# Optimization experiments

Hardware: AMD Instinct MI355X
Metric: run time of the kernel (lower is better)

## Reference

```python
import jax, jax.numpy as jnp
import numpy as np

N = 8192      # num_nodes
E = 262144    # edges (before self loops)
F_IN = 256    # input_dim
H = 4         # nheads
C = 32        # nhid (per-head out channels)
D = H * C     # concat dim = 128
NEG_SLOPE = 0.2
EPS = 1e-5


def setup_inputs() -> dict:
    key = jax.random.key(0)
    ks = jax.random.split(key, 12)
    s = 0.05
    x = jax.random.normal(ks[0], (N, F_IN), jnp.float32)
    adj = jax.random.randint(ks[1], (2, E), 0, N, dtype=jnp.int32)
    Wgat = jax.random.normal(ks[2], (F_IN, D), jnp.float32) * s   # GATConv lin weight
    att_src = jax.random.normal(ks[3], (H, C), jnp.float32) * s
    att_dst = jax.random.normal(ks[4], (H, C), jnp.float32) * s
    bias_gat = jax.random.normal(ks[5], (D,), jnp.float32) * s
    Wq = jax.random.normal(ks[6], (H, D, C), jnp.float32) * s     # per-head selfattention query proj
    Wk = jax.random.normal(ks[7], (H, D, C), jnp.float32) * s     # per-head selfattention key proj
    Wpro = jax.random.normal(ks[8], (D, D), jnp.float32) * s      # prolayer (no bias)
    ln_g = jnp.ones((D,), jnp.float32)
    ln_b = jnp.zeros((D,), jnp.float32)
    return {"x": x, "adj": adj, "Wgat": Wgat, "att_src": att_src,
            "att_dst": att_dst, "bias_gat": bias_gat, "Wq": Wq, "Wk": Wk,
            "Wpro": Wpro, "ln_g": ln_g, "ln_b": ln_b}


def _gat_conv(x, src, dst, Wgat, att_src, att_dst, bias_gat):
    # PyG GATConv, concat=True, add_self_loops handled by caller.
    xw = (x @ Wgat).reshape(N, H, C)                       # [N,H,C]
    a_src = jnp.einsum('nhc,hc->nh', xw, att_src)          # [N,H]
    a_dst = jnp.einsum('nhc,hc->nh', xw, att_dst)
    e = jax.nn.leaky_relu(a_src[src] + a_dst[dst], NEG_SLOPE)  # [Etot,H]
    # segment softmax over incoming edges of each destination node
    m = jax.ops.segment_max(e, dst, num_segments=N)        # [N,H]
    e = jnp.exp(e - m[dst])
    denom = jax.ops.segment_sum(e, dst, num_segments=N)    # [N,H]
    alpha = e / denom[dst]                                 # [Etot,H]
    out = jax.ops.segment_sum(xw[src] * alpha[:, :, None], dst, num_segments=N)
    return out.reshape(N, D) + bias_gat                    # [N,D]


def reference(x, adj, Wgat, att_src, att_dst, bias_gat, Wq, Wk, Wpro, ln_g, ln_b):
    # add self loops (PyG GATConv default)
    loops = jnp.arange(N, dtype=adj.dtype)
    src = jnp.concatenate([adj[0], loops])
    dst = jnp.concatenate([adj[1], loops])

    h_cat = _gat_conv(x, src, dst, Wgat, att_src, att_dst, bias_gat)  # [N,D]
    h = h_cat @ Wpro                                                   # prolayer

    # sum over nheads independent dense node self-attention heads
    q = jnp.einsum('nd,hdc->hnc', h, Wq)                   # [H,N,C]
    k = jnp.einsum('nd,hdc->hnc', h, Wk)
    scores = jnp.einsum('hnc,hmc->hnm', q, k) / jnp.sqrt(jnp.float32(C))  # [H,N,N]
    att = jax.nn.softmax(scores, axis=-1)
    temp = jnp.einsum('hnm,md->nd', att, h)                # sum of per-head att @ h

    y = temp + h                                           # residual
    mu = jnp.mean(y, axis=-1, keepdims=True)
    var = jnp.mean(jnp.square(y - mu), axis=-1, keepdims=True)
    return (y - mu) / jnp.sqrt(var + EPS) * ln_g + ln_b
```

## Files before the change

kernel.cpp:

```cpp
#include <hip/hip_runtime.h>
#include <math.h>

#define N_NODES 8192
#define E_EDGES 262144
#define ETOT (E_EDGES + N_NODES)
#define F_IN 256
#define NH 4
#define NC 32
#define DD 128
#define NEG_SLOPE 0.2f
#define LN_EPS 1e-5f
#define QK_SCALE (1.4426950408889634f / 5.656854249492381f)

typedef __attribute__((ext_vector_type(8))) short bf16x8;
typedef __attribute__((ext_vector_type(4))) float f32x4;

__device__ __forceinline__ float fexp2(float x) { return __builtin_amdgcn_exp2f(x); }
__device__ __forceinline__ float flog2(float x) { return __builtin_amdgcn_logf(x); }
__device__ __forceinline__ float frcp(float x)  { return __builtin_amdgcn_rcpf(x); }

__device__ __forceinline__ unsigned short f2bf(float f) {
    unsigned u = __float_as_uint(f);
    u += 0x7FFFu + ((u >> 16) & 1u);
    return (unsigned short)(u >> 16);
}
__device__ __forceinline__ unsigned pk2bf(float lo, float hi) {
    unsigned a = __float_as_uint(lo) + 0x8000u;
    unsigned b = __float_as_uint(hi) + 0x8000u;
    return __builtin_amdgcn_perm(b, a, 0x07060302u);
}

__global__ __launch_bounds__(256) void k_cvt(const float* __restrict__ Wgat,
                                             const float* __restrict__ Wpro,
                                             const float* __restrict__ Wq,
                                             const float* __restrict__ Wk,
                                             unsigned short* __restrict__ Wgt,
                                             unsigned short* __restrict__ Wpt,
                                             unsigned short* __restrict__ Wqt,
                                             unsigned short* __restrict__ Wkt) {
    int t = blockIdx.x * 256 + threadIdx.x;
    if (t < 32768) {
        int c = t >> 8, k = t & 255;
        Wgt[t] = f2bf(Wgat[(size_t)k * 128 + c]);
    } else if (t < 49152) {
        int i = t - 32768, c = i >> 7, k = i & 127;
        Wpt[i] = f2bf(Wpro[(size_t)k * 128 + c]);
    } else if (t < 65536) {
        int i = t - 49152, h = i >> 12, r = i & 4095, c = r >> 7, k = r & 127;
        Wqt[i] = f2bf(Wq[h * 4096 + k * 32 + c]);
    } else if (t < 81920) {
        int i = t - 65536, h = i >> 12, r = i & 4095, c = r >> 7, k = r & 127;
        Wkt[i] = f2bf(Wk[h * 4096 + k * 32 + c]);
    }
}

__global__ __launch_bounds__(256) void k_gemm_att(const float* __restrict__ x,
                                                  const unsigned short* __restrict__ Wgt,
                                                  const float* __restrict__ att_src,
                                                  const float* __restrict__ att_dst,
                                                  float* __restrict__ xw,
                                                  float* __restrict__ asrc,
                                                  float* __restrict__ adst) {
    __shared__ unsigned short xs[32 * 256];
    const int tid = threadIdx.x;
    const int w = tid >> 6, lane = tid & 63, lq = lane & 15, g = lane >> 4;
    const int n0 = blockIdx.x * 32;
#pragma unroll
    for (int m = 0; m < 4; ++m) {
        int lin = m * 256 + tid;
        int row = lin >> 5, ch = lin & 31;
        const float* src = &x[(size_t)(n0 + row) * 256 + ch * 8];
        float4 v0 = *(const float4*)src;
        float4 v1 = *(const float4*)(src + 4);
        uint4 o;
        o.x = (unsigned)f2bf(v0.x) | ((unsigned)f2bf(v0.y) << 16);
        o.y = (unsigned)f2bf(v0.z) | ((unsigned)f2bf(v0.w) << 16);
        o.z = (unsigned)f2bf(v1.x) | ((unsigned)f2bf(v1.y) << 16);
        o.w = (unsigned)f2bf(v1.z) | ((unsigned)f2bf(v1.w) << 16);
        *(uint4*)&xs[row * 256 + ((ch + row) & 31) * 8] = o;
    }
    __syncthreads();
    f32x4 zero = {0.f, 0.f, 0.f, 0.f};
    f32x4 acc[2][2];
#pragma unroll
    for (int s = 0; s < 2; ++s) { acc[s][0] = zero; acc[s][1] = zero; }
#pragma unroll
    for (int kb = 0; kb < 8; ++kb) {
        bf16x8 af[2], bf[2];
#pragma unroll
        for (int s = 0; s < 2; ++s) {
            int row = s * 16 + lq;
            af[s] = *(const bf16x8*)&xs[row * 256 + (((kb * 4 + g) + row) & 31) * 8];
        }
#pragma unroll
        for (int c = 0; c < 2; ++c)
            bf[c] = *(const bf16x8*)(Wgt + (size_t)(w * 32 + c * 16 + lq) * 256 + kb * 32 + g * 8);
#pragma unroll
        for (int s = 0; s < 2; ++s)
#pragma unroll
            for (int c = 0; c < 2; ++c)
                acc[s][c] = __builtin_amdgcn_mfma_f32_16x16x32_bf16(af[s], bf[c], acc[s][c], 0, 0, 0);
    }
#pragma unroll
    for (int s = 0; s < 2; ++s)
#pragma unroll
        for (int c = 0; c < 2; ++c)
#pragma unroll
            for (int r = 0; r < 4; ++r)
                xw[(size_t)(n0 + s * 16 + 4 * g + r) * DD + w * 32 + c * 16 + lq] = acc[s][c][r];
    float avs0 = att_src[w * 32 + lq],      avd0 = att_dst[w * 32 + lq];
    float avs1 = att_src[w * 32 + 16 + lq], avd1 = att_dst[w * 32 + 16 + lq];
#pragma unroll
    for (int s = 0; s < 2; ++s) {
        f32x4 vs, vd;
#pragma unroll
        for (int r = 0; r < 4; ++r) {
            vs[r] = acc[s][0][r] * avs0 + acc[s][1][r] * avs1;
            vd[r] = acc[s][0][r] * avd0 + acc[s][1][r] * avd1;
        }
#pragma unroll
        for (int off = 1; off < 16; off <<= 1)
#pragma unroll
            for (int r = 0; r < 4; ++r) {
                vs[r] += __shfl_xor(vs[r], off);
                vd[r] += __shfl_xor(vd[r], off);
            }
        if (lq == 0) {
#pragma unroll
            for (int r = 0; r < 4; ++r) {
                asrc[(n0 + s * 16 + 4 * g + r) * 4 + w] = vs[r];
                adst[(n0 + s * 16 + 4 * g + r) * 4 + w] = vd[r];
            }
        }
    }
}

__global__ __launch_bounds__(256) void k_gemm_pro(const float* __restrict__ hcat,
                                                  const unsigned short* __restrict__ Wpt,
                                                  const unsigned short* __restrict__ Wqt,
                                                  const unsigned short* __restrict__ Wkt,
                                                  float* __restrict__ hbuf,
                                                  unsigned short* __restrict__ Htb,
                                                  unsigned short* __restrict__ Qb,
                                                  unsigned short* __restrict__ Kb) {
    __shared__ unsigned short xs[32 * 128];
    __shared__ unsigned short hsd[32 * 128];
    const int tid = threadIdx.x;
    const int w = tid >> 6, lane = tid & 63, lq = lane & 15, g = lane >> 4;
    const int n0 = blockIdx.x * 32;
#pragma unroll
    for (int m = 0; m < 2; ++m) {
        int lin = m * 256 + tid;
        int row = lin >> 4, ch = lin & 15;
        const float* src = &hcat[(size_t)(n0 + row) * 128 + ch * 8];
        float4 v0 = *(const float4*)src;
        float4 v1 = *(const float4*)(src + 4);
        uint4 o;
        o.x = (unsigned)f2bf(v0.x) | ((unsigned)f2bf(v0.y) << 16);
        o.y = (unsigned)f2bf(v0.z) | ((unsigned)f2bf(v0.w) << 16);
        o.z = (unsigned)f2bf(v1.x) | ((unsigned)f2bf(v1.y) << 16);
        o.w = (unsigned)f2bf(v1.z) | ((unsigned)f2bf(v1.w) << 16);
        *(uint4*)&xs[row * 128 + ((ch + row) & 15) * 8] = o;
    }
    __syncthreads();
    f32x4 zero = {0.f, 0.f, 0.f, 0.f};
    f32x4 acc[2][2];
#pragma unroll
    for (int s = 0; s < 2; ++s) { acc[s][0] = zero; acc[s][1] = zero; }
#pragma unroll
    for (int kb = 0; kb < 4; ++kb) {
        bf16x8 af[2], bf[2];
#pragma unroll
        for (int s = 0; s < 2; ++s) {
            int row = s * 16 + lq;
            af[s] = *(const bf16x8*)&xs[row * 128 + (((kb * 4 + g) + row) & 15) * 8];
        }
#pragma unroll
        for (int c = 0; c < 2; ++c)
            bf[c] = *(const bf16x8*)(Wpt + (size_t)(w * 32 + c * 16 + lq) * 128 + kb * 32 + g * 8);
#pragma unroll
        for (int s = 0; s < 2; ++s)
#pragma unroll
            for (int c = 0; c < 2; ++c)
                acc[s][c] = __builtin_amdgcn_mfma_f32_16x16x32_bf16(af[s], bf[c], acc[s][c], 0, 0, 0);
    }
#pragma unroll
    for (int s = 0; s < 2; ++s)
#pragma unroll
        for (int c = 0; c < 2; ++c) {
            int col = w * 32 + c * 16 + lq;
#pragma unroll
            for (int r = 0; r < 4; ++r) {
                int row = s * 16 + 4 * g + r;
                hbuf[(size_t)(n0 + row) * 128 + col] = acc[s][c][r];
                hsd[row * 128 + (((col >> 3) + row) & 15) * 8 + (col & 7)] = f2bf(acc[s][c][r]);
            }
            uint2 hp;
            hp.x = pk2bf(acc[s][c][0], acc[s][c][1]);
            hp.y = pk2bf(acc[s][c][2], acc[s][c][3]);
            *(uint2*)(Htb + (size_t)col * N_NODES + n0 + s * 16 + 4 * g) = hp;
        }
    __syncthreads();
    f32x4 aq[2][2], ak[2][2];
#pragma unroll
    for (int s = 0; s < 2; ++s)
#pragma unroll
        for (int c = 0; c < 2; ++c) { aq[s][c] = zero; ak[s][c] = zero; }
#pragma unroll
    for (int kb = 0; kb < 4; ++kb) {
        bf16x8 af[2], bq[2], bk[2];
#pragma unroll
        for (int s = 0; s < 2; ++s) {
            int row = s * 16 + lq;
            af[s] = *(const bf16x8*)&hsd[row * 128 + (((kb * 4 + g) + row) & 15) * 8];
        }
#pragma unroll
        for (int c = 0; c < 2; ++c) {
            size_t widx = ((size_t)w * 32 + c * 16 + lq) * 128 + kb * 32 + g * 8;
            bq[c] = *(const bf16x8*)(Wqt + widx);
            bk[c] = *(const bf16x8*)(Wkt + widx);
        }
#pragma unroll
        for (int s = 0; s < 2; ++s)
#pragma unroll
            for (int c = 0; c < 2; ++c) {
                aq[s][c] = __builtin_amdgcn_mfma_f32_16x16x32_bf16(af[s], bq[c], aq[s][c], 0, 0, 0);
                ak[s][c] = __builtin_amdgcn_mfma_f32_16x16x32_bf16(af[s], bk[c], ak[s][c], 0, 0, 0);
            }
    }
#pragma unroll
    for (int s = 0; s < 2; ++s)
#pragma unroll
        for (int c = 0; c < 2; ++c)
#pragma unroll
            for (int r = 0; r < 4; ++r) {
                size_t nidx = (size_t)w * N_NODES + n0 + s * 16 + 4 * g + r;
                Qb[nidx * NC + c * 16 + lq] = f2bf(aq[s][c][r] * QK_SCALE);
                Kb[nidx * NC + c * 16 + lq] = f2bf(ak[s][c][r]);
            }
}

__device__ __forceinline__ void edge_sd(int e, const int* adj, int& s, int& d) {
    if (e < E_EDGES) { s = adj[e]; d = adj[E_EDGES + e]; }
    else { s = e - E_EDGES; d = s; }
}

__global__ void k_deg(const int* __restrict__ adj, int* __restrict__ deg) {
    int e = blockIdx.x * blockDim.x + threadIdx.x;
    if (e >= ETOT) return;
    int d = (e < E_EDGES) ? adj[E_EDGES + e] : e - E_EDGES;
    atomicAdd(&deg[d], 1);
}

__global__ __launch_bounds__(1024) void k_scan(const int* __restrict__ deg,
                                               int* __restrict__ rowptr,
                                               int* __restrict__ cursor) {
    __shared__ int sm[1024];
    int t = threadIdx.x;
    int v[8], sum = 0;
#pragma unroll
    for (int j = 0; j < 8; ++j) { v[j] = deg[t * 8 + j]; sum += v[j]; }
    sm[t] = sum;
    __syncthreads();
    for (int off = 1; off < 1024; off <<= 1) {
        int x = (t >= off) ? sm[t - off] : 0;
        __syncthreads();
        sm[t] += x;
        __syncthreads();
    }
    int base = sm[t] - sum;
#pragma unroll
    for (int j = 0; j < 8; ++j) {
        rowptr[t * 8 + j] = base;
        cursor[t * 8 + j] = base;
        base += v[j];
    }
    if (t == 1023) rowptr[8192] = base;
}

__global__ void k_fill(const int* __restrict__ adj, const float* __restrict__ asrc,
                       const float* __restrict__ adst, int* __restrict__ cursor,
                       uint4* __restrict__ rec_csr) {
    int e = blockIdx.x * blockDim.x + threadIdx.x;
    if (e >= ETOT) return;
    int s, d; edge_sd(e, adj, s, d);
    int pos = atomicAdd(&cursor[d], 1);
    float4 as4 = *(const float4*)&asrc[s * 4];
    float4 ad4 = *(const float4*)&adst[d * 4];
    const float L2E = 1.4426950408889634f;
    float v;
    float4 p;
    v = as4.x + ad4.x; v = v > 0.f ? v : NEG_SLOPE * v; p.x = fexp2(v * L2E);
    v = as4.y + ad4.y; v = v > 0.f ? v : NEG_SLOPE * v; p.y = fexp2(v * L2E);
    v = as4.z + ad4.z; v = v > 0.f ? v : NEG_SLOPE * v; p.z = fexp2(v * L2E);
    v = as4.w + ad4.w; v = v > 0.f ? v : NEG_SLOPE * v; p.w = fexp2(v * L2E);
    uint4 rec;
    rec.x = (unsigned)s;
    rec.y = pk2bf(p.x, p.y);
    rec.z = pk2bf(p.z, p.w);
    rec.w = 0u;
    rec_csr[pos] = rec;
}

__global__ __launch_bounds__(256) void k_aggregate(const int* __restrict__ rowptr,
                                                   const uint4* __restrict__ rec_csr,
                                                   const float* __restrict__ xw,
                                                   const float* __restrict__ bias,
                                                   float* __restrict__ hcat) {
    int n = blockIdx.x * 2 + (threadIdx.x >> 7);
    int c = threadIdx.x & 127;
    int h = c >> 5;
    int beg = rowptr[n], end = rowptr[n + 1];
    float acc = 0.f, den = 0.f;
    int i = beg;
    for (; i + 2 <= end; i += 2) {
        uint4 r0 = rec_csr[i], r1 = rec_csr[i + 1];
        unsigned w0 = (h < 2) ? r0.y : r0.z;
        unsigned w1 = (h < 2) ? r1.y : r1.z;
        float p0 = __uint_as_float((h & 1) ? (w0 & 0xFFFF0000u) : (w0 << 16));
        float p1 = __uint_as_float((h & 1) ? (w1 & 0xFFFF0000u) : (w1 << 16));
        den += p0 + p1;
        acc += p0 * xw[(size_t)r0.x * DD + c] + p1 * xw[(size_t)r1.x * DD + c];
    }
    if (i < end) {
        uint4 r0 = rec_csr[i];
        unsigned w0 = (h < 2) ? r0.y : r0.z;
        float p0 = __uint_as_float((h & 1) ? (w0 & 0xFFFF0000u) : (w0 << 16));
        den += p0;
        acc += p0 * xw[(size_t)r0.x * DD + c];
    }
    hcat[(size_t)n * DD + c] = bias[c] + acc * frcp(den);
}

__global__ __launch_bounds__(256) void k_attn_l(const unsigned short* __restrict__ Qb,
                                                const unsigned short* __restrict__ Kb,
                                                float* __restrict__ lsum) {
    const int tid = threadIdx.x;
    const int w = tid >> 6;
    const int lane = tid & 63;
    const int lq = lane & 15;
    const int g = lane >> 4;
    const int q0 = blockIdx.x * 64;
    const int ks = blockIdx.y;
    f32x4 zero = {0.f, 0.f, 0.f, 0.f};

    bf16x8 qf[4];
#pragma unroll
    for (int j = 0; j < 4; ++j)
        qf[j] = *(const bf16x8*)(Qb + ((size_t)w * N_NODES + q0 + j * 16 + lq) * NC + g * 8);
    const unsigned short* Kp = Kb + (size_t)w * N_NODES * NC;

    float l[4] = {0.f, 0.f, 0.f, 0.f};
    for (int kt = 0; kt < 16; ++kt) {
        const int k0 = ks * 1024 + kt * 64;
#pragma unroll
        for (int t = 0; t < 4; ++t) {
            const bf16x8 kf = *(const bf16x8*)(Kp + (size_t)(k0 + t * 16 + lq) * NC + g * 8);
#pragma unroll
            for (int j = 0; j < 4; ++j) {
                f32x4 st = __builtin_amdgcn_mfma_f32_16x16x32_bf16(kf, qf[j], zero, 0, 0, 0);
                l[j] += (fexp2(st[0]) + fexp2(st[1])) + (fexp2(st[2]) + fexp2(st[3]));
            }
        }
    }
#pragma unroll
    for (int j = 0; j < 4; ++j) {
        float lj = l[j];
        lj += __shfl_xor(lj, 16); lj += __shfl_xor(lj, 32);
        if (lane < 16) atomicAdd(&lsum[w * N_NODES + q0 + j * 16 + lq], lj);
    }
}

__global__ __launch_bounds__(256, 2) void k_attn_pv(
        const unsigned short* __restrict__ Qb,
        const unsigned short* __restrict__ Kb,
        const unsigned short* __restrict__ Htb,
        const float* __restrict__ lsum,
        float* __restrict__ Opart) {
    __shared__ unsigned short htl[128 * 64];
    __shared__ unsigned short plds[32 * 64];
    const int tid = threadIdx.x;
    const int w = tid >> 6;
    const int lane = tid & 63;
    const int lq = lane & 15;
    const int g = lane >> 4;
    const int q0 = blockIdx.x * 32;
    const int ks = blockIdx.y;
    const int sd = tid >> 3, sc = tid & 7;
    f32x4 zero = {0.f, 0.f, 0.f, 0.f};

    float lg0[4], lg1[4];
    bf16x8 qreg0[4], qreg1[4];
#pragma unroll
    for (int h = 0; h < 4; ++h) {
        lg0[h] = -flog2(lsum[h * N_NODES + q0 + lq]);
        lg1[h] = -flog2(lsum[h * N_NODES + q0 + 16 + lq]);
        qreg0[h] = *(const bf16x8*)(Qb + ((size_t)h * N_NODES + q0 + lq) * NC + g * 8);
        qreg1[h] = *(const bf16x8*)(Qb + ((size_t)h * N_NODES + q0 + 16 + lq) * NC + g * 8);
    }

    f32x4 acc[2][2];
#pragma unroll
    for (int a = 0; a < 2; ++a) { acc[a][0] = zero; acc[a][1] = zero; }

    const int wch = 2 * w + (g >> 1);
    const int whalf = (g & 1) * 8;

    for (int kt = 0; kt < 16; ++kt) {
        const int k0 = ks * 1024 + kt * 64;
        __syncthreads();
#pragma unroll
        for (int mm = 0; mm < 4; ++mm) {
            int d = mm * 32 + sd;
            uint4 v = *(const uint4*)(Htb + (size_t)d * N_NODES + k0 + sc * 8);
            *(uint4*)&htl[d * 64 + ((sc + d) & 7) * 8] = v;
        }
        f32x4 ps0 = zero, ps1 = zero;
#pragma unroll
        for (int h = 0; h < 4; ++h) {
            const bf16x8 kf = *(const bf16x8*)(Kb + ((size_t)h * N_NODES + k0 + w * 16 + lq) * NC + g * 8);
            f32x4 st0 = __builtin_amdgcn_mfma_f32_16x16x32_bf16(kf, qreg0[h], zero, 0, 0, 0);
            f32x4 st1 = __builtin_amdgcn_mfma_f32_16x16x32_bf16(kf, qreg1[h], zero, 0, 0, 0);
#pragma unroll
            for (int r = 0; r < 4; ++r) {
                ps0[r] += fexp2(st0[r] + lg0[h]);
                ps1[r] += fexp2(st1[r] + lg1[h]);
            }
        }
        uint2 pk;
        pk.x = pk2bf(ps0[0], ps0[1]); pk.y = pk2bf(ps0[2], ps0[3]);
        {
            int row = lq;
            *(uint2*)((char*)plds + row * 128 + ((wch + row) & 7) * 16 + whalf) = pk;
        }
        pk.x = pk2bf(ps1[0], ps1[1]); pk.y = pk2bf(ps1[2], ps1[3]);
        {
            int row = 16 + lq;
            *(uint2*)((char*)plds + row * 128 + ((wch + row) & 7) * 16 + whalf) = pk;
        }
        __syncthreads();
#pragma unroll
        for (int kc = 0; kc < 2; ++kc) {
            int row0 = lq, row1 = 16 + lq;
            const bf16x8 af0 = *(const bf16x8*)((char*)plds + row0 * 128 + ((kc * 4 + g + row0) & 7) * 16);
            const bf16x8 af1 = *(const bf16x8*)((char*)plds + row1 * 128 + ((kc * 4 + g + row1) & 7) * 16);
#pragma unroll
            for (int dl = 0; dl < 2; ++dl) {
                int dd = (w * 2 + dl) * 16 + lq;
                const bf16x8 bf = *(const bf16x8*)&htl[dd * 64 + ((kc * 4 + g + dd) & 7) * 8];
                acc[dl][0] = __builtin_amdgcn_mfma_f32_16x16x32_bf16(af0, bf, acc[dl][0], 0, 0, 0);
                acc[dl][1] = __builtin_amdgcn_mfma_f32_16x16x32_bf16(af1, bf, acc[dl][1], 0, 0, 0);
            }
        }
    }
    const size_t ob = (size_t)ks * N_NODES + q0;
#pragma unroll
    for (int dl = 0; dl < 2; ++dl) {
        int d = (w * 2 + dl) * 16 + lq;
#pragma unroll
        for (int s = 0; s < 2; ++s)
#pragma unroll
            for (int r = 0; r < 4; ++r)
                Opart[(ob + s * 16 + 4 * g + r) * DD + d] = acc[dl][s][r];
    }
}

__global__ __launch_bounds__(128) void k_finalize(const float* __restrict__ Opart,
                                                  const float* __restrict__ hb,
                                                  const float* __restrict__ g,
                                                  const float* __restrict__ b,
                                                  float* __restrict__ out) {
    __shared__ float red[2];
    int n = blockIdx.x, c = threadIdx.x;
    const size_t ND = (size_t)N_NODES * DD;
    size_t idx = (size_t)n * DD + c;
    float y = hb[idx];
#pragma unroll
    for (int i = 0; i < 8; ++i) y += Opart[i * ND + idx];
    float s = y;
#pragma unroll
    for (int off = 1; off < 64; off <<= 1) s += __shfl_xor(s, off);
    if ((c & 63) == 0) red[c >> 6] = s;
    __syncthreads();
    float mu = (red[0] + red[1]) * (1.f / 128.f);
    float dv = y - mu;
    float vs = dv * dv;
#pragma unroll
    for (int off = 1; off < 64; off <<= 1) vs += __shfl_xor(vs, off);
    __syncthreads();
    if ((c & 63) == 0) red[c >> 6] = vs;
    __syncthreads();
    float rstd = rsqrtf((red[0] + red[1]) * (1.f / 128.f) + LN_EPS);
    out[idx] = dv * rstd * g[c] + b[c];
}

extern "C" void kernel_launch(void* const* d_in, const int* in_sizes, int n_in,
                              void* d_out, int out_size, void* d_ws, size_t ws_size,
                              hipStream_t stream) {
    const float* x        = (const float*)d_in[0];
    const int*   adj      = (const int*)d_in[1];
    const float* Wgat     = (const float*)d_in[2];
    const float* att_src  = (const float*)d_in[3];
    const float* att_dst  = (const float*)d_in[4];
    const float* bias_gat = (const float*)d_in[5];
    const float* Wq       = (const float*)d_in[6];
    const float* Wk       = (const float*)d_in[7];
    const float* Wpro     = (const float*)d_in[8];
    const float* ln_g     = (const float*)d_in[9];
    const float* ln_b     = (const float*)d_in[10];
    float* out = (float*)d_out;

    const size_t ND = (size_t)N_NODES * DD;
    unsigned short* Qb  = (unsigned short*)d_ws;
    unsigned short* Kb  = Qb + (1 << 20);
    unsigned short* Htb = Kb + (1 << 20);
    unsigned short* Wgt = Htb + (1 << 20);
    unsigned short* Wpt = Wgt + 32768;
    unsigned short* Wqt = Wpt + 16384;
    unsigned short* Wkt = Wqt + 16384;
    float* xw      = (float*)(Wkt + 16384);
    float* hcat    = xw + ND;
    float* hbuf    = hcat + ND;
    float* asrc    = hbuf + ND;
    float* adst    = asrc + N_NODES * NH;
    float* lsum    = adst + N_NODES * NH;
    int*   deg     = (int*)(lsum + N_NODES * NH);
    int*   rowptr  = deg + 8192;
    int*   cursor  = rowptr + 8704;
    uint4* rec_csr = (uint4*)(cursor + 8704);
    float* Opart   = (float*)(rec_csr + ETOT);

    hipMemsetAsync(lsum, 0, N_NODES * NH * sizeof(float) + N_NODES * sizeof(int), stream);
    k_cvt<<<320, 256, 0, stream>>>(Wgat, Wpro, Wq, Wk, Wgt, Wpt, Wqt, Wkt);
    k_gemm_att<<<N_NODES / 32, 256, 0, stream>>>(x, Wgt, att_src, att_dst, xw, asrc, adst);
    int eblocks = (ETOT + 255) / 256;
    k_deg<<<eblocks, 256, 0, stream>>>(adj, deg);
    k_scan<<<1, 1024, 0, stream>>>(deg, rowptr, cursor);
    k_fill<<<eblocks, 256, 0, stream>>>(adj, asrc, adst, cursor, rec_csr);
    k_aggregate<<<N_NODES / 2, 256, 0, stream>>>(rowptr, rec_csr, xw, bias_gat, hcat);
    k_gemm_pro<<<N_NODES / 32, 256, 0, stream>>>(hcat, Wpt, Wqt, Wkt, hbuf, Htb, Qb, Kb);
    dim3 lgrid(N_NODES / 64, 8);
    k_attn_l<<<lgrid, 256, 0, stream>>>(Qb, Kb, lsum);
    dim3 agrid(N_NODES / 32, 8);
    k_attn_pv<<<agrid, 256, 0, stream>>>(Qb, Kb, Htb, lsum, Opart);
    k_finalize<<<N_NODES, 128, 0, stream>>>(Opart, hbuf, ln_g, ln_b, out);
}
```

Before: 266.0 us.

## Fuse degree count into weight convert, unroll aggregate, replace lsum atomics with partials

Moves the per-edge degree atomic count into the weight-conversion kernel, which removes one launch. It also unrolls the CSR aggregation loop by four with two independent accumulators so more gathers can be in flight. The softmax row-sum atomics in the attention-normaliser kernel become plain stores into eight per-split partial buffers, and the PV kernel sums those partials itself. This shrinks the memset to the degree array only, at the cost of extra workspace and eight extra loads per head in the PV prologue.

```diff
diff --git a/kernel.cpp b/kernel.cpp
--- a/kernel.cpp
+++ b/kernel.cpp
@@ -37,7 +37,9 @@
                                              unsigned short* __restrict__ Wgt,
                                              unsigned short* __restrict__ Wpt,
                                              unsigned short* __restrict__ Wqt,
-                                             unsigned short* __restrict__ Wkt) {
+                                             unsigned short* __restrict__ Wkt,
+                                             const int* __restrict__ adj,
+                                             int* __restrict__ deg) {
     int t = blockIdx.x * 256 + threadIdx.x;
     if (t < 32768) {
         int c = t >> 8, k = t & 255;
@@ -52,6 +54,10 @@
         int i = t - 65536, h = i >> 12, r = i & 4095, c = r >> 7, k = r & 127;
         Wkt[i] = f2bf(Wk[h * 4096 + k * 32 + c]);
     }
+    if (t < ETOT) {
+        int d = (t < E_EDGES) ? adj[E_EDGES + t] : t - E_EDGES;
+        atomicAdd(&deg[d], 1);
+    }
 }
 
 __global__ __launch_bounds__(256) void k_gemm_att(const float* __restrict__ x,
@@ -243,13 +249,6 @@
 __device__ __forceinline__ void edge_sd(int e, const int* adj, int& s, int& d) {
     if (e < E_EDGES) { s = adj[e]; d = adj[E_EDGES + e]; }
     else { s = e - E_EDGES; d = s; }
-}
-
-__global__ void k_deg(const int* __restrict__ adj, int* __restrict__ deg) {
-    int e = blockIdx.x * blockDim.x + threadIdx.x;
-    if (e >= ETOT) return;
-    int d = (e < E_EDGES) ? adj[E_EDGES + e] : e - E_EDGES;
-    atomicAdd(&deg[d], 1);
 }
 
 __global__ __launch_bounds__(1024) void k_scan(const int* __restrict__ deg,
@@ -302,6 +301,11 @@
     rec_csr[pos] = rec;
 }
 
+__device__ __forceinline__ float rec_p(const uint4& r, int h) {
+    unsigned w = (h < 2) ? r.y : r.z;
+    return __uint_as_float((h & 1) ? (w & 0xFFFF0000u) : (w << 16));
+}
+
 __global__ __launch_bounds__(256) void k_aggregate(const int* __restrict__ rowptr,
                                                    const uint4* __restrict__ rec_csr,
                                                    const float* __restrict__ xw,
@@ -311,30 +315,30 @@
     int c = threadIdx.x & 127;
     int h = c >> 5;
     int beg = rowptr[n], end = rowptr[n + 1];
-    float acc = 0.f, den = 0.f;
+    float acc0 = 0.f, acc1 = 0.f, den0 = 0.f, den1 = 0.f;
     int i = beg;
-    for (; i + 2 <= end; i += 2) {
+    for (; i + 4 <= end; i += 4) {
         uint4 r0 = rec_csr[i], r1 = rec_csr[i + 1];
-        unsigned w0 = (h < 2) ? r0.y : r0.z;
-        unsigned w1 = (h < 2) ? r1.y : r1.z;
-        float p0 = __uint_as_float((h & 1) ? (w0 & 0xFFFF0000u) : (w0 << 16));
-        float p1 = __uint_as_float((h & 1) ? (w1 & 0xFFFF0000u) : (w1 << 16));
-        den += p0 + p1;
-        acc += p0 * xw[(size_t)r0.x * DD + c] + p1 * xw[(size_t)r1.x * DD + c];
-    }
-    if (i < end) {
+        uint4 r2 = rec_csr[i + 2], r3 = rec_csr[i + 3];
+        float p0 = rec_p(r0, h), p1 = rec_p(r1, h);
+        float p2 = rec_p(r2, h), p3 = rec_p(r3, h);
+        den0 += p0 + p1;
+        den1 += p2 + p3;
+        acc0 += p0 * xw[(size_t)r0.x * DD + c] + p1 * xw[(size_t)r1.x * DD + c];
+        acc1 += p2 * xw[(size_t)r2.x * DD + c] + p3 * xw[(size_t)r3.x * DD + c];
+    }
+    for (; i < end; ++i) {
         uint4 r0 = rec_csr[i];
-        unsigned w0 = (h < 2) ? r0.y : r0.z;
-        float p0 = __uint_as_float((h & 1) ? (w0 & 0xFFFF0000u) : (w0 << 16));
-        den += p0;
-        acc += p0 * xw[(size_t)r0.x * DD + c];
-    }
-    hcat[(size_t)n * DD + c] = bias[c] + acc * frcp(den);
+        float p0 = rec_p(r0, h);
+        den0 += p0;
+        acc0 += p0 * xw[(size_t)r0.x * DD + c];
+    }
+    hcat[(size_t)n * DD + c] = bias[c] + (acc0 + acc1) * frcp(den0 + den1);
 }
 
 __global__ __launch_bounds__(256) void k_attn_l(const unsigned short* __restrict__ Qb,
                                                 const unsigned short* __restrict__ Kb,
-                                                float* __restrict__ lsum) {
+                                                float* __restrict__ lpart) {
     const int tid = threadIdx.x;
     const int w = tid >> 6;
     const int lane = tid & 63;
@@ -367,7 +371,8 @@
     for (int j = 0; j < 4; ++j) {
         float lj = l[j];
         lj += __shfl_xor(lj, 16); lj += __shfl_xor(lj, 32);
-        if (lane < 16) atomicAdd(&lsum[w * N_NODES + q0 + j * 16 + lq], lj);
+        if (lane < 16)
+            lpart[((size_t)ks * NH + w) * N_NODES + q0 + j * 16 + lq] = lj;
     }
 }
 
@@ -375,7 +380,7 @@
         const unsigned short* __restrict__ Qb,
         const unsigned short* __restrict__ Kb,
         const unsigned short* __restrict__ Htb,
-        const float* __restrict__ lsum,
+        const float* __restrict__ lpart,
         float* __restrict__ Opart) {
     __shared__ unsigned short htl[128 * 64];
     __shared__ unsigned short plds[32 * 64];
@@ -393,8 +398,14 @@
     bf16x8 qreg0[4], qreg1[4];
 #pragma unroll
     for (int h = 0; h < 4; ++h) {
-        lg0[h] = -flog2(lsum[h * N_NODES + q0 + lq]);
-        lg1[h] = -flog2(lsum[h * N_NODES + q0 + 16 + lq]);
+        float s0 = 0.f, s1 = 0.f;
+#pragma unroll
+        for (int s = 0; s < 8; ++s) {
+            s0 += lpart[((size_t)s * NH + h) * N_NODES + q0 + lq];
+            s1 += lpart[((size_t)s * NH + h) * N_NODES + q0 + 16 + lq];
+        }
+        lg0[h] = -flog2(s0);
+        lg1[h] = -flog2(s1);
         qreg0[h] = *(const bf16x8*)(Qb + ((size_t)h * N_NODES + q0 + lq) * NC + g * 8);
         qreg1[h] = *(const bf16x8*)(Qb + ((size_t)h * N_NODES + q0 + 16 + lq) * NC + g * 8);
     }
@@ -523,25 +534,25 @@
     float* hbuf    = hcat + ND;
     float* asrc    = hbuf + ND;
     float* adst    = asrc + N_NODES * NH;
-    float* lsum    = adst + N_NODES * NH;
-    int*   deg     = (int*)(lsum + N_NODES * NH);
+    float* lpart   = adst + N_NODES * NH;
+    int*   deg     = (int*)(lpart + 8 * NH * N_NODES);
     int*   rowptr  = deg + 8192;
     int*   cursor  = rowptr + 8704;
     uint4* rec_csr = (uint4*)(cursor + 8704);
     float* Opart   = (float*)(rec_csr + ETOT);
 
-    hipMemsetAsync(lsum, 0, N_NODES * NH * sizeof(float) + N_NODES * sizeof(int), stream);
-    k_cvt<<<320, 256, 0, stream>>>(Wgat, Wpro, Wq, Wk, Wgt, Wpt, Wqt, Wkt);
+    hipMemsetAsync(deg, 0, N_NODES * sizeof(int), stream);
+    int cvtblocks = (ETOT + 255) / 256;
+    k_cvt<<<cvtblocks, 256, 0, stream>>>(Wgat, Wpro, Wq, Wk, Wgt, Wpt, Wqt, Wkt, adj, deg);
     k_gemm_att<<<N_NODES / 32, 256, 0, stream>>>(x, Wgt, att_src, att_dst, xw, asrc, adst);
+    k_scan<<<1, 1024, 0, stream>>>(deg, rowptr, cursor);
     int eblocks = (ETOT + 255) / 256;
-    k_deg<<<eblocks, 256, 0, stream>>>(adj, deg);
-    k_scan<<<1, 1024, 0, stream>>>(deg, rowptr, cursor);
     k_fill<<<eblocks, 256, 0, stream>>>(adj, asrc, adst, cursor, rec_csr);
     k_aggregate<<<N_NODES / 2, 256, 0, stream>>>(rowptr, rec_csr, xw, bias_gat, hcat);
     k_gemm_pro<<<N_NODES / 32, 256, 0, stream>>>(hcat, Wpt, Wqt, Wkt, hbuf, Htb, Qb, Kb);
     dim3 lgrid(N_NODES / 64, 8);
-    k_attn_l<<<lgrid, 256, 0, stream>>>(Qb, Kb, lsum);
+    k_attn_l<<<lgrid, 256, 0, stream>>>(Qb, Kb, lpart);
     dim3 agrid(N_NODES / 32, 8);
-    k_attn_pv<<<agrid, 256, 0, stream>>>(Qb, Kb, Htb, lsum, Opart);
+    k_attn_pv<<<agrid, 256, 0, stream>>>(Qb, Kb, Htb, lpart, Opart);
     k_finalize<<<N_NODES, 128, 0, stream>>>(Opart, hbuf, ln_g, ln_b, out);
 }
```

New measurement: 269.5 us. Within noise of the previous version (+1.3%).
